# Optimization experiments

Measured on AMD Instinct MI355X. Metric: run time of the kernel, lower is better.

The kernel has to match this reference:

```python
import jax, jax.numpy as jnp
import numpy as np
import math

D_MODEL = 1024
D_STATE = 64
BATCH = 16
LENGTH = 4096


def _hippo_legs(n_dim: int) -> np.ndarray:
    """HiPPO-LegS matrix, scaled by 0.5 as in the torch module."""
    n = np.arange(n_dim)[:, None].astype(np.float32)
    k = np.arange(n_dim)[None, :].astype(np.float32)
    a = np.where(n > k, -np.sqrt(2.0 * n + 1.0) * np.sqrt(2.0 * k + 1.0), 0.0)
    a = a + np.diag(-(np.arange(n_dim, dtype=np.float32) + 1.0))
    return (a * 0.5).astype(np.float32)


def setup_inputs() -> dict:
    key = jax.random.key(0)
    k_u, k_B, k_C, k_dt = jax.random.split(key, 4)
    u = jax.random.normal(k_u, (BATCH, LENGTH, D_MODEL), dtype=jnp.float32)
    A = jnp.asarray(_hippo_legs(D_STATE))
    B = jax.random.normal(k_B, (D_STATE, D_MODEL), dtype=jnp.float32) * 0.01
    C = jax.random.normal(k_C, (D_MODEL, D_STATE), dtype=jnp.float32) * 0.01
    D = jnp.ones((D_MODEL,), dtype=jnp.float32)
    log_dt = (jax.random.uniform(k_dt, (D_MODEL,), dtype=jnp.float32)
              * (math.log(0.1) - math.log(0.001)) + math.log(0.001))
    return {"u": u, "A": A, "B": B, "C": C, "D": D, "log_dt": log_dt}


def reference(u, A, B, C, D, log_dt):
    # u: (B, L, d_model)
    d_state = A.shape[0]
    dt_mean = jnp.exp(log_dt).mean()
    a_bar = jnp.eye(d_state, dtype=u.dtype) + dt_mean * A  # (N, N)
    # Precompute input projection for every timestep: (L, B, N)
    bu = jnp.einsum('bld,nd->lbn', u, dt_mean * B)

    def step(x, bu_t):
        # x: (B, N); x_{t} = x_{t-1} @ a_bar.T + (u_t @ b_bar.T)
        x = x @ a_bar.T + bu_t
        return x, x

    x0 = jnp.zeros((u.shape[0], d_state), dtype=u.dtype)
    _, xs = jax.lax.scan(step, x0, bu)  # xs: (L, B, N)
    y = jnp.einsum('lbn,dn->bld', xs, C) + u * D  # (B, L, d_model)
    return y
```

## Files before the change

kernel.cpp:

```cpp
#include <hip/hip_runtime.h>


#define DM   1024
#define DS   64
#define NB   16
#define LL   4096
#define LC   64
#define NCH  (LL / LC)
#define MTOT (NB * LL)
#define NTASK (NB * NCH)

#define WS_ABAR 64
#define WS_A2   4160
#define WS_APOW 8256
#define WS_TMP  12352
#define WS_E    16448
#define WS_S    (WS_E + NTASK * DS)
#define WS_BHI  (WS_S + NTASK * DS)
#define WS_CHI  (WS_BHI + 32768)
#define WS_XS   (WS_CHI + 32768)
#define WS_BU   (WS_XS + 2097152)

typedef __attribute__((ext_vector_type(4))) float f32x4;
typedef __attribute__((ext_vector_type(8))) short bf16x8;
typedef __attribute__((ext_vector_type(8))) unsigned short ushort8;

__device__ inline unsigned short bf16_rne(float f) {
    unsigned u = __builtin_bit_cast(unsigned, f);
    u += 0x7FFFu + ((u >> 16) & 1u);
    return (unsigned short)(u >> 16);
}

__global__ __launch_bounds__(256) void k_prep(const float* __restrict__ A,
                                              const float* __restrict__ log_dt,
                                              float* __restrict__ ws) {
    __shared__ float red[256];
    int tid = threadIdx.x;
    float s = 0.f;
    for (int i = tid; i < DM; i += 256) s += expf(log_dt[i]);
    red[tid] = s;
    __syncthreads();
    for (int off = 128; off > 0; off >>= 1) {
        if (tid < off) red[tid] += red[tid + off];
        __syncthreads();
    }
    float dt = red[0] * (1.f / (float)DM);
    if (tid == 0) ws[0] = dt;
    for (int idx = tid; idx < 4096; idx += 256) {
        int n = idx >> 6, m = idx & 63;
        ws[WS_ABAR + idx] = dt * A[idx] + ((n == m) ? 1.f : 0.f);
    }
}

__global__ __launch_bounds__(256) void k_cvt(const float* __restrict__ Bm,
                                             const float* __restrict__ C,
                                             float* __restrict__ ws) {
    int bid = blockIdx.x;
    int isC = bid >> 6;
    const float* src = isC ? C : Bm;
    unsigned short* dst = (unsigned short*)(ws + (isC ? WS_CHI : WS_BHI));
    float scale = isC ? 1.f : ws[0];
    int i = ((bid & 63) * 256 + threadIdx.x) * 4;
    float4 v = *reinterpret_cast<const float4*>(&src[i]);
    ushort4 h;
    h.x = bf16_rne(v.x * scale);
    h.y = bf16_rne(v.y * scale);
    h.z = bf16_rne(v.z * scale);
    h.w = bf16_rne(v.w * scale);
    *reinterpret_cast<ushort4*>(&dst[i]) = h;
}

__global__ __launch_bounds__(256) void k_matsq(const float* __restrict__ src,
                                               float* __restrict__ dst) {
    __shared__ float s[64][65];
    int tid = threadIdx.x;
#pragma unroll
    for (int rep = 0; rep < 16; ++rep) {
        int idx = rep * 256 + tid;
        s[idx >> 6][idx & 63] = src[idx];
    }
    __syncthreads();
    int n = (blockIdx.x << 2) + (tid >> 6);
    int m = tid & 63;
    float a0 = 0.f, a1 = 0.f, a2 = 0.f, a3 = 0.f;
#pragma unroll
    for (int k = 0; k < 64; k += 4) {
        a0 = fmaf(s[n][k + 0], s[k + 0][m], a0);
        a1 = fmaf(s[n][k + 1], s[k + 1][m], a1);
        a2 = fmaf(s[n][k + 2], s[k + 2][m], a2);
        a3 = fmaf(s[n][k + 3], s[k + 3][m], a3);
    }
    dst[(n << 6) + m] = (a0 + a1) + (a2 + a3);
}

__global__ __launch_bounds__(256, 4) void k_gemm1(const float* __restrict__ u,
                                                  const float* __restrict__ ws,
                                                  float* __restrict__ bu) {
    __shared__ short a_t[64][72];
    __shared__ short b_t[64][72];
    const unsigned short* bhig = (const unsigned short*)(ws + WS_BHI);
    int tid = threadIdx.x;
    int m0 = blockIdx.x * 64;
    int wid = tid >> 6, lane = tid & 63;
    int lr = lane & 15, lg = lane >> 4;
    int sr = tid >> 3, sc8 = (tid & 7) << 3;
    int bn = tid >> 3, bk8 = (tid & 7) << 3;

    f32x4 acc[4];
#pragma unroll
    for (int j = 0; j < 4; ++j) acc[j] = (f32x4)(0.f);

    float4 ra[2][2];
    ushort8 rb[2];
#pragma unroll
    for (int i = 0; i < 2; ++i) {
        ra[i][0] = *reinterpret_cast<const float4*>(&u[(size_t)(m0 + sr + 32 * i) * DM + sc8]);
        ra[i][1] = *reinterpret_cast<const float4*>(&u[(size_t)(m0 + sr + 32 * i) * DM + sc8 + 4]);
    }
#pragma unroll
    for (int j = 0; j < 2; ++j)
        rb[j] = *reinterpret_cast<const ushort8*>(&bhig[(size_t)(bn + 32 * j) * DM + bk8]);

    for (int kt = 0; kt < 16; ++kt) {
#pragma unroll
        for (int i = 0; i < 2; ++i) {
            ushort8 h;
            h[0] = bf16_rne(ra[i][0].x); h[1] = bf16_rne(ra[i][0].y);
            h[2] = bf16_rne(ra[i][0].z); h[3] = bf16_rne(ra[i][0].w);
            h[4] = bf16_rne(ra[i][1].x); h[5] = bf16_rne(ra[i][1].y);
            h[6] = bf16_rne(ra[i][1].z); h[7] = bf16_rne(ra[i][1].w);
            *reinterpret_cast<ushort8*>(&a_t[sr + 32 * i][sc8]) = h;
        }
#pragma unroll
        for (int j = 0; j < 2; ++j)
            *reinterpret_cast<ushort8*>(&b_t[bn + 32 * j][bk8]) = rb[j];
        __syncthreads();
        if (kt + 1 < 16) {
            int k0n = (kt + 1) * 64;
#pragma unroll
            for (int i = 0; i < 2; ++i) {
                ra[i][0] = *reinterpret_cast<const float4*>(&u[(size_t)(m0 + sr + 32 * i) * DM + k0n + sc8]);
                ra[i][1] = *reinterpret_cast<const float4*>(&u[(size_t)(m0 + sr + 32 * i) * DM + k0n + sc8 + 4]);
            }
#pragma unroll
            for (int j = 0; j < 2; ++j)
                rb[j] = *reinterpret_cast<const ushort8*>(&bhig[(size_t)(bn + 32 * j) * DM + k0n + bk8]);
        }
#pragma unroll
        for (int kf = 0; kf < 2; ++kf) {
            int kb = kf * 32 + lg * 8;
            bf16x8 af = *reinterpret_cast<bf16x8*>(&a_t[wid * 16 + lr][kb]);
#pragma unroll
            for (int nf = 0; nf < 4; ++nf) {
                bf16x8 bf_ = *reinterpret_cast<bf16x8*>(&b_t[nf * 16 + lr][kb]);
                acc[nf] = __builtin_amdgcn_mfma_f32_16x16x32_bf16(af, bf_, acc[nf], 0, 0, 0);
            }
        }
        __syncthreads();
    }
#pragma unroll
    for (int nf = 0; nf < 4; ++nf)
#pragma unroll
        for (int q = 0; q < 4; ++q) {
            size_t row = (size_t)(m0 + wid * 16 + lg * 4 + q);
            bu[row * DS + nf * 16 + lr] = acc[nf][q];
        }
}

template <int PASS>
__global__ __launch_bounds__(256) void k_scan(float* __restrict__ ws) {
    const float* Abar = ws + WS_ABAR;
    const float* A2m  = ws + WS_A2;
    float* bu = ws + WS_BU;
    unsigned short* xs = (unsigned short*)(ws + WS_XS);
    int tid = threadIdx.x;
    int w = tid >> 6, lane = tid & 63;
    int task = blockIdx.x * 4 + w;
    __shared__ float xbuf[4][64];
    __shared__ float bbuf[4][2][64];

    float a_row[64], a2_row[64];
#pragma unroll
    for (int mg = 0; mg < 16; ++mg) {
        float4 v = *reinterpret_cast<const float4*>(&Abar[lane * 64 + mg * 4]);
        a_row[mg * 4 + 0] = v.x; a_row[mg * 4 + 1] = v.y;
        a_row[mg * 4 + 2] = v.z; a_row[mg * 4 + 3] = v.w;
        float4 v2 = *reinterpret_cast<const float4*>(&A2m[lane * 64 + mg * 4]);
        a2_row[mg * 4 + 0] = v2.x; a2_row[mg * 4 + 1] = v2.y;
        a2_row[mg * 4 + 2] = v2.z; a2_row[mg * 4 + 3] = v2.w;
    }
    float x;
    if (PASS == 0) x = 0.f;
    else           x = ws[WS_S + (size_t)task * DS + lane];

    size_t r0 = (size_t)(task >> 6) * LL + (size_t)(task & 63) * LC;
    float* bub = bu + r0 * DS;
    unsigned short* xp = xs + r0 * DS;

    float b0v = bub[lane];
    float b1v = bub[DS + lane];
    bbuf[w][0][lane] = b0v;
    asm volatile("" ::: "memory");

    for (int i = 0; i < 32; ++i) {
        float nb0 = bub[(2 * i + 2) * DS + lane];
        float nb1 = bub[(2 * i + 3) * DS + lane];
        xbuf[w][lane] = x;
        asm volatile("" ::: "memory");
        float* bb = &bbuf[w][i & 1][0];
        float bp[4];
#pragma unroll
        for (int g = 0; g < 4; ++g) {
            float acc = 0.f;
#pragma unroll
            for (int q = 0; q < 4; ++q) {
                float4 bm = *reinterpret_cast<float4*>(&bb[g * 16 + q * 4]);
                acc = fmaf(a_row[g * 16 + q * 4 + 0], bm.x, acc);
                acc = fmaf(a_row[g * 16 + q * 4 + 1], bm.y, acc);
                acc = fmaf(a_row[g * 16 + q * 4 + 2], bm.z, acc);
                acc = fmaf(a_row[g * 16 + q * 4 + 3], bm.w, acc);
            }
            bp[g] = acc;
        }
        float bdot = ((bp[0] + bp[1]) + (bp[2] + bp[3])) + b1v;
        float p2[4], p1d[4];
#pragma unroll
        for (int g = 0; g < 4; ++g) {
            float acc2 = 0.f, acc1 = 0.f;
#pragma unroll
            for (int q = 0; q < 4; ++q) {
                float4 xm = *reinterpret_cast<float4*>(&xbuf[w][g * 16 + q * 4]);
                float c20 = a2_row[g * 16 + q * 4 + 0], c21 = a2_row[g * 16 + q * 4 + 1];
                float c22 = a2_row[g * 16 + q * 4 + 2], c23 = a2_row[g * 16 + q * 4 + 3];
                acc2 = fmaf(c20, xm.x, acc2);
                acc2 = fmaf(c21, xm.y, acc2);
                acc2 = fmaf(c22, xm.z, acc2);
                acc2 = fmaf(c23, xm.w, acc2);
                if (PASS == 1) {
                    float c10 = a_row[g * 16 + q * 4 + 0], c11 = a_row[g * 16 + q * 4 + 1];
                    float c12 = a_row[g * 16 + q * 4 + 2], c13 = a_row[g * 16 + q * 4 + 3];
                    acc1 = fmaf(c10, xm.x, acc1);
                    acc1 = fmaf(c11, xm.y, acc1);
                    acc1 = fmaf(c12, xm.z, acc1);
                    acc1 = fmaf(c13, xm.w, acc1);
                }
            }
            p2[g] = acc2; p1d[g] = acc1;
        }
        float xe = ((p2[0] + p2[1]) + (p2[2] + p2[3])) + bdot;
        if (PASS == 1) {
            float xo = ((p1d[0] + p1d[1]) + (p1d[2] + p1d[3])) + b0v;
            xp[(2 * i) * DS + lane] = bf16_rne(xo);
            xp[(2 * i + 1) * DS + lane] = bf16_rne(xe);
        }
        asm volatile("" ::: "memory");
        bbuf[w][(i + 1) & 1][lane] = nb0;
        b0v = nb0; b1v = nb1; x = xe;
    }
    if (PASS == 0) ws[WS_E + (size_t)task * DS + lane] = x;
}

__global__ __launch_bounds__(64) void k_combine(float* __restrict__ ws) {
    const float* Apow = ws + WS_APOW;
    int b = blockIdx.x;
    int lane = threadIdx.x;
    __shared__ float xbuf[64];
    __shared__ float e_lds[NCH][64];
    const float* Eb = ws + WS_E + (size_t)b * NCH * DS;
#pragma unroll
    for (int r = 0; r < 16; ++r) {
        int idx = r * 64 + lane;
        int jj = idx >> 4, c4 = (idx & 15) << 2;
        *reinterpret_cast<float4*>(&e_lds[jj][c4]) =
            *reinterpret_cast<const float4*>(&Eb[jj * DS + c4]);
    }
    float p_row[64];
#pragma unroll
    for (int mg = 0; mg < 16; ++mg) {
        float4 v = *reinterpret_cast<const float4*>(&Apow[lane * 64 + mg * 4]);
        p_row[mg * 4 + 0] = v.x; p_row[mg * 4 + 1] = v.y;
        p_row[mg * 4 + 2] = v.z; p_row[mg * 4 + 3] = v.w;
    }
    __syncthreads();
    float x = 0.f;
    for (int jj = 0; jj < NCH; ++jj) {
        size_t task = (size_t)b * NCH + jj;
        ws[WS_S + task * DS + lane] = x;
        float e = e_lds[jj][lane];
        xbuf[lane] = x;
        asm volatile("" ::: "memory");
        float part[4];
#pragma unroll
        for (int g = 0; g < 4; ++g) {
            float acc = (g == 0) ? e : 0.f;
#pragma unroll
            for (int q = 0; q < 4; ++q) {
                float4 xm = *reinterpret_cast<float4*>(&xbuf[g * 16 + q * 4]);
                acc = fmaf(p_row[g * 16 + q * 4 + 0], xm.x, acc);
                acc = fmaf(p_row[g * 16 + q * 4 + 1], xm.y, acc);
                acc = fmaf(p_row[g * 16 + q * 4 + 2], xm.z, acc);
                acc = fmaf(p_row[g * 16 + q * 4 + 3], xm.w, acc);
            }
            part[g] = acc;
        }
        asm volatile("" ::: "memory");
        x = (part[0] + part[1]) + (part[2] + part[3]);
    }
}

__global__ __launch_bounds__(256, 4) void k_gemm2(const float* __restrict__ u,
                                                  const float* __restrict__ Dv,
                                                  const float* __restrict__ ws,
                                                  float* __restrict__ y) {
    __shared__ __align__(16) char smem[2 * 128 * 72 * 2];
    short (*a_t)[72] = (short(*)[72])(smem);
    short (*c_t)[72] = (short(*)[72])(smem + 18432);
    float (*out_lds)[132] = (float(*)[132])(smem);

    const unsigned short* xsb = (const unsigned short*)(ws + WS_XS);
    const unsigned short* chig = (const unsigned short*)(ws + WS_CHI);
    int tid = threadIdx.x;
    int m0 = blockIdx.x * 128;
    int d0 = blockIdx.y * 128;
    int wid = tid >> 6, lane = tid & 63;
    int lr = lane & 15, lg = lane >> 4;

#pragma unroll
    for (int rep = 0; rep < 4; ++rep) {
        int idx = rep * 256 + tid;
        int r = idx >> 3, k8 = (idx & 7) << 3;
        *reinterpret_cast<ushort8*>(&a_t[r][k8]) =
            *reinterpret_cast<const ushort8*>(&xsb[(size_t)(m0 + r) * DS + k8]);
    }
#pragma unroll
    for (int rep = 0; rep < 4; ++rep) {
        int idx = rep * 256 + tid;
        int dl = idx >> 3, n8 = (idx & 7) << 3;
        *reinterpret_cast<ushort8*>(&c_t[dl][n8]) =
            *reinterpret_cast<const ushort8*>(&chig[(size_t)(d0 + dl) * DS + n8]);
    }
    __syncthreads();

    f32x4 acc[2][8];
#pragma unroll
    for (int i = 0; i < 2; ++i)
#pragma unroll
        for (int j = 0; j < 8; ++j) acc[i][j] = (f32x4)(0.f);

#pragma unroll
    for (int kf = 0; kf < 2; ++kf) {
        int kb = kf * 32 + lg * 8;
        bf16x8 ah0 = *reinterpret_cast<bf16x8*>(&a_t[wid * 32 + lr][kb]);
        bf16x8 ah1 = *reinterpret_cast<bf16x8*>(&a_t[wid * 32 + 16 + lr][kb]);
#pragma unroll
        for (int nf = 0; nf < 8; ++nf) {
            bf16x8 cb = *reinterpret_cast<bf16x8*>(&c_t[nf * 16 + lr][kb]);
            acc[0][nf] = __builtin_amdgcn_mfma_f32_16x16x32_bf16(ah0, cb, acc[0][nf], 0, 0, 0);
            acc[1][nf] = __builtin_amdgcn_mfma_f32_16x16x32_bf16(ah1, cb, acc[1][nf], 0, 0, 0);
        }
    }
    __syncthreads();

#pragma unroll
    for (int h = 0; h < 2; ++h) {
        if ((wid >> 1) == h) {
            int rbase = (wid & 1) * 32;
#pragma unroll
            for (int mf = 0; mf < 2; ++mf)
#pragma unroll
                for (int nf = 0; nf < 8; ++nf)
#pragma unroll
                    for (int q = 0; q < 4; ++q)
                        out_lds[rbase + mf * 16 + lg * 4 + q][nf * 16 + lr] = acc[mf][nf][q];
        }
        __syncthreads();
#pragma unroll
        for (int rep = 0; rep < 8; ++rep) {
            int idx = rep * 256 + tid;
            int r = idx >> 5, c4 = (idx & 31) << 2;
            float4 a = *reinterpret_cast<float4*>(&out_lds[r][c4]);
            size_t row = (size_t)(m0 + h * 64 + r);
            int c = d0 + c4;
            float4 uv = *reinterpret_cast<const float4*>(&u[row * DM + c]);
            float4 dv = *reinterpret_cast<const float4*>(&Dv[c]);
            float4 o;
            o.x = a.x + uv.x * dv.x;
            o.y = a.y + uv.y * dv.y;
            o.z = a.z + uv.z * dv.z;
            o.w = a.w + uv.w * dv.w;
            *reinterpret_cast<float4*>(&y[row * DM + c]) = o;
        }
        if (h == 0) __syncthreads();
    }
}

extern "C" void kernel_launch(void* const* d_in, const int* in_sizes, int n_in,
                              void* d_out, int out_size, void* d_ws, size_t ws_size,
                              hipStream_t stream) {
    (void)in_sizes; (void)n_in; (void)out_size; (void)ws_size;
    const float* u      = (const float*)d_in[0];
    const float* A      = (const float*)d_in[1];
    const float* Bm     = (const float*)d_in[2];
    const float* C      = (const float*)d_in[3];
    const float* Dv     = (const float*)d_in[4];
    const float* log_dt = (const float*)d_in[5];
    float* y  = (float*)d_out;
    float* ws = (float*)d_ws;
    float* bu = ws + WS_BU;

    k_prep<<<dim3(1), dim3(256), 0, stream>>>(A, log_dt, ws);
    k_cvt<<<dim3(128), dim3(256), 0, stream>>>(Bm, C, ws);
    k_matsq<<<dim3(16), dim3(256), 0, stream>>>(ws + WS_ABAR, ws + WS_A2);
    k_matsq<<<dim3(16), dim3(256), 0, stream>>>(ws + WS_A2,   ws + WS_APOW);
    k_matsq<<<dim3(16), dim3(256), 0, stream>>>(ws + WS_APOW, ws + WS_TMP);
    k_matsq<<<dim3(16), dim3(256), 0, stream>>>(ws + WS_TMP,  ws + WS_APOW);
    k_matsq<<<dim3(16), dim3(256), 0, stream>>>(ws + WS_APOW, ws + WS_TMP);
    k_matsq<<<dim3(16), dim3(256), 0, stream>>>(ws + WS_TMP,  ws + WS_APOW);

    k_gemm1<<<dim3(MTOT / 64), dim3(256), 0, stream>>>(u, ws, bu);
    k_scan<0><<<dim3(NTASK / 4), dim3(256), 0, stream>>>(ws);
    k_combine<<<dim3(NB), dim3(64), 0, stream>>>(ws);
    k_scan<1><<<dim3(NTASK / 4), dim3(256), 0, stream>>>(ws);
    k_gemm2<<<dim3(MTOT / 128, DM / 128), dim3(256), 0, stream>>>(u, Dv, ws, y);
}
```

Before: 336.8 us.

## Fuse prep and convert kernels; load u directly into MFMA registers in gemm1

The dt reduction, Abar construction and B/C bf16 conversion now run in a single launch, with every block recomputing the dt mean redundantly, which removes one kernel launch. In gemm1 each lane loads its u fragment straight from global memory in MFMA operand layout, dropping the u shared-memory tile. The B tile is now double-buffered in LDS, which removes one barrier per k-step. The direct u loads are 32-byte per-lane row segments, so coalescing may be worse than the previous tiled load.

```diff
diff --git a/kernel.cpp b/kernel.cpp
--- a/kernel.cpp
+++ b/kernel.cpp
@@ -31,11 +31,14 @@
     return (unsigned short)(u >> 16);
 }
 
-__global__ __launch_bounds__(256) void k_prep(const float* __restrict__ A,
-                                              const float* __restrict__ log_dt,
-                                              float* __restrict__ ws) {
+__global__ __launch_bounds__(256) void k_setup(const float* __restrict__ A,
+                                               const float* __restrict__ Bm,
+                                               const float* __restrict__ C,
+                                               const float* __restrict__ log_dt,
+                                               float* __restrict__ ws) {
     __shared__ float red[256];
     int tid = threadIdx.x;
+    int bid = blockIdx.x;
     float s = 0.f;
     for (int i = tid; i < DM; i += 256) s += expf(log_dt[i]);
     red[tid] = s;
@@ -45,29 +48,27 @@
         __syncthreads();
     }
     float dt = red[0] * (1.f / (float)DM);
-    if (tid == 0) ws[0] = dt;
-    for (int idx = tid; idx < 4096; idx += 256) {
-        int n = idx >> 6, m = idx & 63;
-        ws[WS_ABAR + idx] = dt * A[idx] + ((n == m) ? 1.f : 0.f);
-    }
-}
-
-__global__ __launch_bounds__(256) void k_cvt(const float* __restrict__ Bm,
-                                             const float* __restrict__ C,
-                                             float* __restrict__ ws) {
-    int bid = blockIdx.x;
-    int isC = bid >> 6;
-    const float* src = isC ? C : Bm;
-    unsigned short* dst = (unsigned short*)(ws + (isC ? WS_CHI : WS_BHI));
-    float scale = isC ? 1.f : ws[0];
-    int i = ((bid & 63) * 256 + threadIdx.x) * 4;
-    float4 v = *reinterpret_cast<const float4*>(&src[i]);
-    ushort4 h;
-    h.x = bf16_rne(v.x * scale);
-    h.y = bf16_rne(v.y * scale);
-    h.z = bf16_rne(v.z * scale);
-    h.w = bf16_rne(v.w * scale);
-    *reinterpret_cast<ushort4*>(&dst[i]) = h;
+
+    if (bid < 128) {
+        int isC = bid >> 6;
+        const float* src = isC ? C : Bm;
+        unsigned short* dst = (unsigned short*)(ws + (isC ? WS_CHI : WS_BHI));
+        float scale = isC ? 1.f : dt;
+        int i = ((bid & 63) * 256 + tid) * 4;
+        float4 v = *reinterpret_cast<const float4*>(&src[i]);
+        ushort4 h;
+        h.x = bf16_rne(v.x * scale);
+        h.y = bf16_rne(v.y * scale);
+        h.z = bf16_rne(v.z * scale);
+        h.w = bf16_rne(v.w * scale);
+        *reinterpret_cast<ushort4*>(&dst[i]) = h;
+    } else {
+        if (tid == 0) ws[0] = dt;
+        for (int idx = tid; idx < 4096; idx += 256) {
+            int n = idx >> 6, m = idx & 63;
+            ws[WS_ABAR + idx] = dt * A[idx] + ((n == m) ? 1.f : 0.f);
+        }
+    }
 }
 
 __global__ __launch_bounds__(256) void k_matsq(const float* __restrict__ src,
@@ -96,67 +97,67 @@
 __global__ __launch_bounds__(256, 4) void k_gemm1(const float* __restrict__ u,
                                                   const float* __restrict__ ws,
                                                   float* __restrict__ bu) {
-    __shared__ short a_t[64][72];
-    __shared__ short b_t[64][72];
+    __shared__ short b_t[2][64][72];
     const unsigned short* bhig = (const unsigned short*)(ws + WS_BHI);
     int tid = threadIdx.x;
     int m0 = blockIdx.x * 64;
     int wid = tid >> 6, lane = tid & 63;
     int lr = lane & 15, lg = lane >> 4;
-    int sr = tid >> 3, sc8 = (tid & 7) << 3;
     int bn = tid >> 3, bk8 = (tid & 7) << 3;
 
+    const float* urow = u + (size_t)(m0 + wid * 16 + lr) * DM + lg * 8;
+
     f32x4 acc[4];
 #pragma unroll
     for (int j = 0; j < 4; ++j) acc[j] = (f32x4)(0.f);
 
-    float4 ra[2][2];
+    float4 ua[2][2];
     ushort8 rb[2];
 #pragma unroll
-    for (int i = 0; i < 2; ++i) {
-        ra[i][0] = *reinterpret_cast<const float4*>(&u[(size_t)(m0 + sr + 32 * i) * DM + sc8]);
-        ra[i][1] = *reinterpret_cast<const float4*>(&u[(size_t)(m0 + sr + 32 * i) * DM + sc8 + 4]);
+    for (int kf = 0; kf < 2; ++kf) {
+        ua[kf][0] = *reinterpret_cast<const float4*>(&urow[kf * 32]);
+        ua[kf][1] = *reinterpret_cast<const float4*>(&urow[kf * 32 + 4]);
     }
 #pragma unroll
     for (int j = 0; j < 2; ++j)
         rb[j] = *reinterpret_cast<const ushort8*>(&bhig[(size_t)(bn + 32 * j) * DM + bk8]);
 
     for (int kt = 0; kt < 16; ++kt) {
-#pragma unroll
-        for (int i = 0; i < 2; ++i) {
+        int cur = kt & 1;
+#pragma unroll
+        for (int j = 0; j < 2; ++j)
+            *reinterpret_cast<ushort8*>(&b_t[cur][bn + 32 * j][bk8]) = rb[j];
+        bf16x8 af[2];
+#pragma unroll
+        for (int kf = 0; kf < 2; ++kf) {
             ushort8 h;
-            h[0] = bf16_rne(ra[i][0].x); h[1] = bf16_rne(ra[i][0].y);
-            h[2] = bf16_rne(ra[i][0].z); h[3] = bf16_rne(ra[i][0].w);
-            h[4] = bf16_rne(ra[i][1].x); h[5] = bf16_rne(ra[i][1].y);
-            h[6] = bf16_rne(ra[i][1].z); h[7] = bf16_rne(ra[i][1].w);
-            *reinterpret_cast<ushort8*>(&a_t[sr + 32 * i][sc8]) = h;
-        }
-#pragma unroll
-        for (int j = 0; j < 2; ++j)
-            *reinterpret_cast<ushort8*>(&b_t[bn + 32 * j][bk8]) = rb[j];
-        __syncthreads();
+            h[0] = bf16_rne(ua[kf][0].x); h[1] = bf16_rne(ua[kf][0].y);
+            h[2] = bf16_rne(ua[kf][0].z); h[3] = bf16_rne(ua[kf][0].w);
+            h[4] = bf16_rne(ua[kf][1].x); h[5] = bf16_rne(ua[kf][1].y);
+            h[6] = bf16_rne(ua[kf][1].z); h[7] = bf16_rne(ua[kf][1].w);
+            af[kf] = __builtin_bit_cast(bf16x8, h);
+        }
         if (kt + 1 < 16) {
             int k0n = (kt + 1) * 64;
 #pragma unroll
-            for (int i = 0; i < 2; ++i) {
-                ra[i][0] = *reinterpret_cast<const float4*>(&u[(size_t)(m0 + sr + 32 * i) * DM + k0n + sc8]);
-                ra[i][1] = *reinterpret_cast<const float4*>(&u[(size_t)(m0 + sr + 32 * i) * DM + k0n + sc8 + 4]);
+            for (int kf = 0; kf < 2; ++kf) {
+                ua[kf][0] = *reinterpret_cast<const float4*>(&urow[k0n + kf * 32]);
+                ua[kf][1] = *reinterpret_cast<const float4*>(&urow[k0n + kf * 32 + 4]);
             }
 #pragma unroll
             for (int j = 0; j < 2; ++j)
                 rb[j] = *reinterpret_cast<const ushort8*>(&bhig[(size_t)(bn + 32 * j) * DM + k0n + bk8]);
         }
+        __syncthreads();
 #pragma unroll
         for (int kf = 0; kf < 2; ++kf) {
             int kb = kf * 32 + lg * 8;
-            bf16x8 af = *reinterpret_cast<bf16x8*>(&a_t[wid * 16 + lr][kb]);
 #pragma unroll
             for (int nf = 0; nf < 4; ++nf) {
-                bf16x8 bf_ = *reinterpret_cast<bf16x8*>(&b_t[nf * 16 + lr][kb]);
-                acc[nf] = __builtin_amdgcn_mfma_f32_16x16x32_bf16(af, bf_, acc[nf], 0, 0, 0);
+                bf16x8 bf_ = *reinterpret_cast<bf16x8*>(&b_t[cur][nf * 16 + lr][kb]);
+                acc[nf] = __builtin_amdgcn_mfma_f32_16x16x32_bf16(af[kf], bf_, acc[nf], 0, 0, 0);
             }
         }
-        __syncthreads();
     }
 #pragma unroll
     for (int nf = 0; nf < 4; ++nf)
@@ -408,8 +409,7 @@
     float* ws = (float*)d_ws;
     float* bu = ws + WS_BU;
 
-    k_prep<<<dim3(1), dim3(256), 0, stream>>>(A, log_dt, ws);
-    k_cvt<<<dim3(128), dim3(256), 0, stream>>>(Bm, C, ws);
+    k_setup<<<dim3(129), dim3(256), 0, stream>>>(A, Bm, C, log_dt, ws);
     k_matsq<<<dim3(16), dim3(256), 0, stream>>>(ws + WS_ABAR, ws + WS_A2);
     k_matsq<<<dim3(16), dim3(256), 0, stream>>>(ws + WS_A2,   ws + WS_APOW);
     k_matsq<<<dim3(16), dim3(256), 0, stream>>>(ws + WS_APOW, ws + WS_TMP);
```

Result: faster. 329.5 us (-2.2%).
